# Optimization experiments

Hardware: AMD Instinct MI355X
Metric: run time of the kernel (lower is better)

## Reference

```python
import jax, jax.numpy as jnp
import numpy as np

N = 100000          # nodes
E = 1600000         # directed edges (before self-loops)
IN_FEATS = 128
HID = 16            # per-head hidden of conv1
HEADS = 8
OUT_FEATS = 128     # conv2 output (heads=1, concat=False)
K = 8               # kernel_size
M = 64              # out_channels
NEG_SLOPE_ATT = 0.2 # GATConv negative_slope
NEG_SLOPE_ACT = 0.01  # F.leaky_relu default between convs


def setup_inputs() -> dict:
    key = jax.random.key(0)
    ks = jax.random.split(key, 12)
    s = 0.1
    return {
        "x": jax.random.normal(ks[0], (N, IN_FEATS), jnp.float32),
        "edge_index": jax.random.randint(ks[1], (2, E), 0, N),
        "W1": jax.random.normal(ks[2], (IN_FEATS, HEADS * HID), jnp.float32) * s,
        "att_src1": jax.random.normal(ks[3], (HEADS, HID), jnp.float32) * s,
        "att_dst1": jax.random.normal(ks[4], (HEADS, HID), jnp.float32) * s,
        "b1": jnp.zeros((HEADS * HID,), jnp.float32),
        "W2": jax.random.normal(ks[5], (HEADS * HID, OUT_FEATS), jnp.float32) * s,
        "att_src2": jax.random.normal(ks[6], (1, OUT_FEATS), jnp.float32) * s,
        "att_dst2": jax.random.normal(ks[7], (1, OUT_FEATS), jnp.float32) * s,
        "b2": jnp.zeros((OUT_FEATS,), jnp.float32),
        "g": jax.random.normal(ks[8], (OUT_FEATS, M * K), jnp.float32) * s,
        "mu": jax.random.normal(ks[9], (K, M), jnp.float32) * s,
    }


def gat_conv(x, src, dst, W, att_src, att_dst, bias, n, heads, out_ch):
    # x: [N, F_in]; src/dst: [E'] (self-loops already appended)
    h = (x @ W).reshape(n, heads, out_ch)                 # [N, H, C]
    a_src = jnp.sum(h * att_src[None], axis=-1)           # [N, H]
    a_dst = jnp.sum(h * att_dst[None], axis=-1)           # [N, H]
    e = jax.nn.leaky_relu(a_src[src] + a_dst[dst], NEG_SLOPE_ATT)  # [E', H]
    # segment softmax over destination node (every node has a self-loop)
    e_max = jax.ops.segment_max(e, dst, num_segments=n)   # [N, H]
    e_exp = jnp.exp(e - e_max[dst])
    denom = jax.ops.segment_sum(e_exp, dst, num_segments=n)
    alpha = e_exp / (denom[dst] + 1e-16)                  # [E', H]
    msg = h[src] * alpha[:, :, None]                      # [E', H, C]
    out = jax.ops.segment_sum(msg, dst, num_segments=n)   # [N, H, C]
    return out.reshape(n, heads * out_ch) + bias


def reference(x, edge_index, W1, att_src1, att_dst1, b1,
              W2, att_src2, att_dst2, b2, g, mu):
    n = x.shape[0]
    loops = jnp.arange(n, dtype=edge_index.dtype)
    src = jnp.concatenate([edge_index[0], loops])
    dst = jnp.concatenate([edge_index[1], loops])

    h = gat_conv(x, src, dst, W1, att_src1, att_dst1, b1, n, HEADS, HID)
    h = jax.nn.leaky_relu(h, NEG_SLOPE_ACT)
    h = gat_conv(h, src, dst, W2, att_src2, att_dst2, b2, n, 1, OUT_FEATS)

    out = (h @ g).reshape(n, K, M)                        # [N, K, M]
    eps = 1e-8
    num = jnp.sum(mu[None] * out, axis=-1)                # [N, K]
    den = (jnp.maximum(jnp.linalg.norm(mu, axis=-1), eps)[None]
           * jnp.maximum(jnp.linalg.norm(out, axis=-1), eps))
    return num / den                                      # [N, K]
```

## Files before the change

### kernel.cpp

```cpp
#include <hip/hip_runtime.h>
#include <hip/hip_bf16.h>

typedef short short8 __attribute__((ext_vector_type(8)));
typedef float f32x4 __attribute__((ext_vector_type(4)));

__device__ __forceinline__ float lrelu(float x, float s) { return x > 0.f ? x : x * s; }

__device__ __forceinline__ unsigned short f2bf(float x) {
  union { __hip_bfloat16 b; unsigned short u; } cv;
  cv.b = __float2bfloat16(x);
  return cv.u;
}
__device__ __forceinline__ float bf2f(unsigned short u) {
  return __uint_as_float(((unsigned int)u) << 16);
}

__global__ void __launch_bounds__(256)
prep_kernel(const float* __restrict__ g, unsigned short* __restrict__ gt,
            const float* __restrict__ W1, const float* __restrict__ as1,
            const float* __restrict__ ad1, unsigned short* __restrict__ wt1,
            unsigned short* __restrict__ vt1,
            const float* __restrict__ W2, const float* __restrict__ as2,
            const float* __restrict__ ad2, unsigned short* __restrict__ wt2,
            unsigned short* __restrict__ vt2,
            const float* __restrict__ mu, unsigned short* __restrict__ gmt)
{
  __shared__ float ts[32][68];
  __shared__ float ss[2][128], sd[2][128];
  __shared__ float msq[8];
  const int b = blockIdx.x;
  const int t = threadIdx.x;
  if (b < 32) {
    const int kb = (b >> 3) * 32;
    const int cb = (b & 7) * 64;
    {
      const int r = t >> 3;
      const int c = (t & 7) * 8;
      float4 v0 = *(const float4*)&g[(size_t)(kb + r) * 512 + cb + c];
      float4 v1 = *(const float4*)&g[(size_t)(kb + r) * 512 + cb + c + 4];
      *(float4*)&ts[r][c] = v0;
      *(float4*)&ts[r][c + 4] = v1;
    }
    __syncthreads();
    {
      const int c = t >> 2;
      const int k0 = (t & 3) * 8;
      unsigned short pk[8];
      #pragma unroll
      for (int j = 0; j < 8; ++j) pk[j] = f2bf(ts[k0 + j][c]);
      *(short8*)&gt[(size_t)(cb + c) * 128 + kb + k0] = *(short8*)pk;
    }
  } else if (b < 160) {
    const int isW2 = (b >= 96) ? 1 : 0;
    const float* W  = isW2 ? W2 : W1;
    const float* as = isW2 ? as2 : as1;
    const float* ad = isW2 ? ad2 : ad1;
    unsigned short* wt = isW2 ? wt2 : wt1;
    unsigned short* vt = isW2 ? vt2 : vt1;
    const int HEADS = isW2 ? 1 : 8;
    const int kk = t >> 7;
    const int c  = t & 127;
    const int k  = ((b - (isW2 ? 96 : 32)) << 1) + kk;
    const float wv = W[k * 128 + c];
    wt[c * 128 + k] = f2bf(wv);
    ss[kk][c] = wv * as[c];
    sd[kk][c] = wv * ad[c];
    __syncthreads();
    if (c < 16) {
      const int C = 128 / HEADS;
      const int h = (c < 8) ? c : c - 8;
      float s = 0.f;
      if (h < HEADS) {
        const float* sb = (c < 8) ? ss[kk] : sd[kk];
        for (int j = 0; j < C; ++j) s += sb[h * C + j];
      }
      vt[c * 128 + k] = f2bf(s);
    }
  } else {
    if (t < 8) {
      float s = 0.f;
      for (int m = 0; m < 64; ++m) { const float v = mu[t * 64 + m]; s += v * v; }
      msq[t] = fmaxf(sqrtf(s), 1e-8f);
    }
    __syncthreads();
    #pragma unroll
    for (int p = 0; p < 4; ++p) {
      const int idx = t + p * 256;
      const int j = idx >> 3, k = idx & 7;
      float s = 0.f;
      for (int m = 0; m < 64; ++m) s += mu[k * 64 + m] * g[(size_t)j * 512 + k * 64 + m];
      gmt[k * 128 + j] = f2bf(s / msq[k]);
      gmt[(8 + (idx >> 7)) * 128 + (idx & 127)] = 0;
    }
  }
}

__global__ void __launch_bounds__(256)
deg_count_kernel(const int* __restrict__ edst, int* __restrict__ deg, int E, int n) {
  const int grp = blockIdx.x & 3;
  const int lo = (int)(((long long)n * grp) >> 2);
  const int hi = (int)(((long long)n * (grp + 1)) >> 2);
  const int tid = (blockIdx.x >> 2) * blockDim.x + threadIdx.x;
  const int stride = (gridDim.x >> 2) * blockDim.x;
  for (int i = tid; i < E; i += stride) {
    const int d = edst[i];
    if (d >= lo && d < hi) atomicAdd(&deg[d], 1);
  }
}

__global__ void __launch_bounds__(256)
scan1_kernel(const int* __restrict__ deg, int* __restrict__ out,
             int* __restrict__ blksum, int n) {
  __shared__ int ts[256];
  const int t = threadIdx.x;
  const int base = blockIdx.x * 2048 + t * 8;
  int v[8]; int s = 0;
  #pragma unroll
  for (int i = 0; i < 8; ++i) {
    int x = (base + i < n) ? deg[base + i] + 1 : 0;
    v[i] = s; s += x;
  }
  ts[t] = s;
  __syncthreads();
  for (int off = 1; off < 256; off <<= 1) {
    int add = (t >= off) ? ts[t - off] : 0;
    __syncthreads();
    ts[t] += add;
    __syncthreads();
  }
  const int excl = ts[t] - s;
  #pragma unroll
  for (int i = 0; i < 8; ++i)
    if (base + i < n) out[base + i] = excl + v[i];
  if (t == 255) blksum[blockIdx.x] = ts[255];
}

__global__ void scan2_kernel(int* __restrict__ blksum, int nb) {
  const int t = threadIdx.x;
  int v = (t < nb) ? blksum[t] : 0;
  #pragma unroll
  for (int off = 1; off < 64; off <<= 1) {
    int u = __shfl_up(v, off);
    if (t >= off) v += u;
  }
  if (t < nb) blksum[t] = v;
}

__global__ void scan3_kernel(int* __restrict__ out, const int* __restrict__ blksum, int n) {
  int i = blockIdx.x * blockDim.x + threadIdx.x;
  if (i >= n) return;
  int b = i >> 11;
  if (b > 0) out[i] += blksum[b - 1];
}

__global__ void __launch_bounds__(256)
scatter_kernel(const int* __restrict__ esrc, const int* __restrict__ edst,
               int* __restrict__ rowptr, int* __restrict__ col,
               int E, int n) {
  const int grp = blockIdx.x & 3;
  const int lo = (int)(((long long)n * grp) >> 2);
  const int hi = (int)(((long long)n * (grp + 1)) >> 2);
  const int tid = (blockIdx.x >> 2) * blockDim.x + threadIdx.x;
  const int stride = (gridDim.x >> 2) * blockDim.x;
  const int Etot = E + n;
  for (int i = tid; i < Etot; i += stride) {
    int s, d;
    if (i < E) { s = esrc[i]; d = edst[i]; } else { s = d = i - E; }
    if (d >= lo && d < hi) {
      int p = atomicAdd(&rowptr[d], 1);
      col[p] = s;
    }
  }
}

template<int HEADS, bool BF16IN, bool I8OUT>
__global__ void __launch_bounds__(256)
feat_mfma_kernel(const void* __restrict__ In_, const unsigned short* __restrict__ wt,
                 const unsigned short* __restrict__ vt, const float* __restrict__ bias_in,
                 void* __restrict__ Hout_, float* __restrict__ hscale,
                 float* __restrict__ a_src, float* __restrict__ a_dst, int n)
{
  __shared__ unsigned short xs[64][136];
  const int t = threadIdx.x;
  const int w = t >> 6, lane = t & 63;
  const int l15 = lane & 15, lg = lane >> 4;
  const int nbase = blockIdx.x << 6;

  {
    const int r = t >> 2;
    const int c0s = (t & 3) << 5;
    const int node = nbase + r;
    if (BF16IN) {
      const unsigned short* In2 = (const unsigned short*)In_;
      #pragma unroll
      for (int i = 0; i < 4; ++i) {
        unsigned short pk[8];
        if (node < n) {
          short8 v = *(const short8*)&In2[(size_t)node * 128 + c0s + i * 8];
          #pragma unroll
          for (int j = 0; j < 8; ++j) {
            float f = bf2f((unsigned short)v[j]) + bias_in[c0s + i * 8 + j];
            pk[j] = f2bf(lrelu(f, 0.01f));
          }
        } else {
          #pragma unroll
          for (int j = 0; j < 8; ++j) pk[j] = 0;
        }
        *(short8*)&xs[r][c0s + i * 8] = *(short8*)pk;
      }
    } else {
      const float* In1 = (const float*)In_;
      #pragma unroll
      for (int i = 0; i < 8; ++i) {
        unsigned short pk[4];
        if (node < n) {
          float4 v = *(const float4*)&In1[(size_t)node * 128 + c0s + i * 4];
          pk[0] = f2bf(v.x); pk[1] = f2bf(v.y); pk[2] = f2bf(v.z); pk[3] = f2bf(v.w);
        } else { pk[0] = pk[1] = pk[2] = pk[3] = 0; }
        *(uint2*)&xs[r][c0s + i * 4] = *(uint2*)pk;
      }
    }
  }
  __syncthreads();

  short8 afr[4];
  #pragma unroll
  for (int kc = 0; kc < 4; ++kc)
    afr[kc] = *(const short8*)&xs[w * 16 + l15][kc * 32 + lg * 8];

  const unsigned short* bp[9];
  #pragma unroll
  for (int ct = 0; ct < 8; ++ct)
    bp[ct] = wt + (size_t)(ct * 16 + l15) * 128 + lg * 8;
  bp[8] = vt + (size_t)l15 * 128 + lg * 8;

  f32x4 acc[9];
  #pragma unroll
  for (int ct = 0; ct < 9; ++ct) acc[ct] = (f32x4){0.f, 0.f, 0.f, 0.f};

  short8 bcur[9], bnxt[9];
  #pragma unroll
  for (int ct = 0; ct < 9; ++ct) bcur[ct] = *(const short8*)bp[ct];

  #pragma unroll
  for (int kc = 0; kc < 4; ++kc) {
    if (kc < 3) {
      #pragma unroll
      for (int ct = 0; ct < 9; ++ct)
        bnxt[ct] = *(const short8*)(bp[ct] + (kc + 1) * 32);
    }
    #pragma unroll
    for (int ct = 0; ct < 9; ++ct)
      acc[ct] = __builtin_amdgcn_mfma_f32_16x16x32_bf16(afr[kc], bcur[ct], acc[ct], 0, 0, 0);
    if (kc < 3) {
      #pragma unroll
      for (int ct = 0; ct < 9; ++ct) bcur[ct] = bnxt[ct];
    }
  }
  __syncthreads();

  if (I8OUT) {
    unsigned char* xb = (unsigned char*)xs;
    float inv127[4], scl[4];
    #pragma unroll
    for (int r = 0; r < 4; ++r) {
      float m = 0.f;
      #pragma unroll
      for (int ct = 0; ct < 8; ++ct) m = fmaxf(m, fabsf(acc[ct][r]));
      m = fmaxf(m, __shfl_xor(m, 1));
      m = fmaxf(m, __shfl_xor(m, 2));
      m = fmaxf(m, __shfl_xor(m, 4));
      m = fmaxf(m, __shfl_xor(m, 8));
      m = fmaxf(m, 1e-12f);
      inv127[r] = 127.f / m;
      scl[r] = m * (1.f / 127.f);
    }
    #pragma unroll
    for (int ct = 0; ct < 8; ++ct)
      #pragma unroll
      for (int r = 0; r < 4; ++r) {
        const int q = __float2int_rn(acc[ct][r] * inv127[r]);
        xb[(w * 16 + lg * 4 + r) * 272 + ct * 16 + l15] = (unsigned char)q;
      }
    if (l15 == 0) {
      #pragma unroll
      for (int r = 0; r < 4; ++r) {
        const int node = nbase + w * 16 + lg * 4 + r;
        if (node < n) hscale[node] = scl[r];
      }
    }
    __syncthreads();
    {
      const int rr = t >> 2;
      const int cc = (t & 3) * 32;
      const int node = nbase + rr;
      if (node < n) {
        unsigned char* H8 = (unsigned char*)Hout_;
        *(uint4*)&H8[(size_t)node * 128 + cc]      = *(const uint4*)&xb[rr * 272 + cc];
        *(uint4*)&H8[(size_t)node * 128 + cc + 16] = *(const uint4*)&xb[rr * 272 + cc + 16];
      }
    }
  } else {
    #pragma unroll
    for (int ct = 0; ct < 8; ++ct)
      #pragma unroll
      for (int r = 0; r < 4; ++r)
        xs[w * 16 + lg * 4 + r][ct * 16 + l15] = f2bf(acc[ct][r]);
    __syncthreads();
    {
      const int r = t >> 2;
      const int c0s = (t & 3) << 5;
      const int node = nbase + r;
      if (node < n) {
        unsigned short* Hb = (unsigned short*)Hout_;
        #pragma unroll
        for (int i = 0; i < 4; ++i)
          *(short8*)&Hb[(size_t)node * 128 + c0s + i * 8] = *(const short8*)&xs[r][c0s + i * 8];
      }
    }
  }

  #pragma unroll
  for (int r = 0; r < 4; ++r) {
    const int node = nbase + w * 16 + lg * 4 + r;
    if (node < n) {
      const float v = acc[8][r];
      if (HEADS == 8) {
        if (l15 < 8) a_src[node * 8 + l15] = v;
        else         a_dst[node * 8 + (l15 - 8)] = v;
      } else {
        if (l15 == 0) a_src[node] = v;
        else if (l15 == 8) a_dst[node] = v;
      }
    }
  }
}

template<int HEADS, bool I8H>
__global__ void __launch_bounds__(256)
agg_csr_kernel(const int* __restrict__ rowptr_end, const int* __restrict__ col,
               const float* __restrict__ a_src, const float* __restrict__ a_dst,
               const void* __restrict__ Hf_, const float* __restrict__ hscale,
               unsigned int* __restrict__ agg, int n)
{
  const int wave = threadIdx.x >> 6;
  const int lane = threadIdx.x & 63;
  const int d = blockIdx.x * 4 + wave;
  if (d >= n) return;
  const int beg = (d == 0) ? 0 : rowptr_end[d - 1];
  const int end = rowptr_end[d];

  const int ei = lane >> 3;
  const int hh = (HEADS == 8) ? (lane & 7) : 0;
  const int bh = (HEADS == 8) ? (lane >> 3) : 0;
  const float adv = (HEADS == 8) ? a_dst[d * 8 + hh] : a_dst[d];
  const unsigned int* Hu = (const unsigned int*)Hf_;
  const unsigned short* H16 = (const unsigned short*)Hf_;

  float accx = 0.f, accy = 0.f, sum = 0.f;
  const int nb8 = (end - beg) >> 3;
  int sv = 0; float a = 0.f, Sv = 0.f;
  if (nb8 > 0) {
    sv = col[beg + ei];
    a = __expf(lrelu(a_src[sv * HEADS + hh] + adv, 0.2f));
    if (I8H) Sv = hscale[sv];
    if (HEADS == 8 || (lane & 7) == 0) sum += a;
  }
  for (int b = 0; b < nb8; ++b) {
    int s[8]; float al[8];
    #pragma unroll
    for (int e = 0; e < 8; ++e) {
      s[e]  = __shfl(sv, e * 8);
      al[e] = __shfl(a, e * 8 + bh);
      if (I8H) al[e] *= __shfl(Sv, e * 8);
    }
    unsigned int hv[8];
    if (I8H) {
      #pragma unroll
      for (int e = 0; e < 8; ++e) hv[e] = H16[(size_t)s[e] * 64 + lane];
    } else {
      #pragma unroll
      for (int e = 0; e < 8; ++e) hv[e] = Hu[(size_t)s[e] * 64 + lane];
    }
    if (b + 1 < nb8) {
      sv = col[beg + ((b + 1) << 3) + ei];
      a = __expf(lrelu(a_src[sv * HEADS + hh] + adv, 0.2f));
      if (I8H) Sv = hscale[sv];
      if (HEADS == 8 || (lane & 7) == 0) sum += a;
    }
    #pragma unroll
    for (int e = 0; e < 8; ++e) {
      if (I8H) {
        const int wv = (int)hv[e];
        accx += al[e] * (float)((wv << 24) >> 24);
        accy += al[e] * (float)((wv << 16) >> 24);
      } else {
        accx += al[e] * __uint_as_float(hv[e] << 16);
        accy += al[e] * __uint_as_float(hv[e] & 0xffff0000u);
      }
    }
  }
  {
    const int p0 = beg + (nb8 << 3);
    const int cnt = end - p0;
    if (cnt > 0) {
      int svt = 0; float at = 0.f, Svt = 0.f;
      if (ei < cnt) {
        svt = col[p0 + ei];
        at = __expf(lrelu(a_src[svt * HEADS + hh] + adv, 0.2f));
        if (I8H) Svt = hscale[svt];
        if (HEADS == 8 || (lane & 7) == 0) sum += at;
      }
      for (int e = 0; e < cnt; ++e) {
        float al = __shfl(at, e * 8 + bh);
        if (I8H) al *= __shfl(Svt, e * 8);
        const int sx = __shfl(svt, e * 8);
        if (I8H) {
          const int wv = (int)H16[(size_t)sx * 64 + lane];
          accx += al * (float)((wv << 24) >> 24);
          accy += al * (float)((wv << 16) >> 24);
        } else {
          const unsigned int hv = Hu[(size_t)sx * 64 + lane];
          accx += al * __uint_as_float(hv << 16);
          accy += al * __uint_as_float(hv & 0xffff0000u);
        }
      }
    }
  }
  sum += __shfl_xor(sum, 8);
  sum += __shfl_xor(sum, 16);
  sum += __shfl_xor(sum, 32);
  const float denom = __shfl(sum, bh) + 1e-16f;
  const float inv = 1.f / denom;
  agg[(size_t)d * 64 + lane] = (unsigned int)f2bf(accx * inv) | ((unsigned int)f2bf(accy * inv) << 16);
}

__global__ void __launch_bounds__(256)
final_kernel(const unsigned short* __restrict__ agg2b, const float* __restrict__ b2,
             const unsigned short* __restrict__ gt, const unsigned short* __restrict__ gmt,
             float* __restrict__ outp, int n)
{
  __shared__ unsigned short os[32][136];
  const int t = threadIdx.x;
  const int w = t >> 6;
  const int lane = t & 63;
  const int l15 = lane & 15;
  const int lg = lane >> 4;
  const int nbase = blockIdx.x << 5;

  {
    const int r = t >> 3;
    const int c = (t & 7) * 16;
    const int node = nbase + r;
    unsigned short pk[16];
    if (node < n) {
      short8 v0 = *(const short8*)&agg2b[(size_t)node * 128 + c];
      short8 v1 = *(const short8*)&agg2b[(size_t)node * 128 + c + 8];
      #pragma unroll
      for (int j = 0; j < 8; ++j) pk[j]     = f2bf(bf2f((unsigned short)v0[j]) + b2[c + j]);
      #pragma unroll
      for (int j = 0; j < 8; ++j) pk[8 + j] = f2bf(bf2f((unsigned short)v1[j]) + b2[c + 8 + j]);
    } else {
      #pragma unroll
      for (int i = 0; i < 16; ++i) pk[i] = 0;
    }
    *(short8*)&os[r][c]     = *(short8*)&pk[0];
    *(short8*)&os[r][c + 8] = *(short8*)&pk[8];
  }
  __syncthreads();

  short8 afr[2][4];
  #pragma unroll
  for (int rt = 0; rt < 2; ++rt)
    #pragma unroll
    for (int kc = 0; kc < 4; ++kc)
      afr[rt][kc] = *(const short8*)&os[rt * 16 + l15][kc * 32 + lg * 8];

  const unsigned short* gw  = gt  + (size_t)(w * 128 + l15) * 128 + lg * 8;
  const unsigned short* gmw = gmt + (size_t)l15 * 128 + lg * 8;

  f32x4 acc[2][8];
  f32x4 accg[2];
  #pragma unroll
  for (int rt = 0; rt < 2; ++rt) {
    #pragma unroll
    for (int ct = 0; ct < 8; ++ct)
      acc[rt][ct] = (f32x4){0.f, 0.f, 0.f, 0.f};
    accg[rt] = (f32x4){0.f, 0.f, 0.f, 0.f};
  }

  short8 bcur[9], bnxt[9];
  #pragma unroll
  for (int ct = 0; ct < 8; ++ct)
    bcur[ct] = *(const short8*)&gw[(size_t)ct * 2048];
  bcur[8] = *(const short8*)gmw;

  #pragma unroll
  for (int kc = 0; kc < 4; ++kc) {
    if (kc < 3) {
      #pragma unroll
      for (int ct = 0; ct < 8; ++ct)
        bnxt[ct] = *(const short8*)&gw[(size_t)ct * 2048 + (kc + 1) * 32];
      bnxt[8] = *(const short8*)(gmw + (kc + 1) * 32);
    }
    #pragma unroll
    for (int ct = 0; ct < 8; ++ct) {
      acc[0][ct] = __builtin_amdgcn_mfma_f32_16x16x32_bf16(afr[0][kc], bcur[ct], acc[0][ct], 0, 0, 0);
      acc[1][ct] = __builtin_amdgcn_mfma_f32_16x16x32_bf16(afr[1][kc], bcur[ct], acc[1][ct], 0, 0, 0);
    }
    accg[0] = __builtin_amdgcn_mfma_f32_16x16x32_bf16(afr[0][kc], bcur[8], accg[0], 0, 0, 0);
    accg[1] = __builtin_amdgcn_mfma_f32_16x16x32_bf16(afr[1][kc], bcur[8], accg[1], 0, 0, 0);
    if (kc < 3) {
      #pragma unroll
      for (int ct = 0; ct < 9; ++ct) bcur[ct] = bnxt[ct];
    }
  }

  const int k0 = w * 2, k1 = w * 2 + 1;
  #pragma unroll
  for (int rt = 0; rt < 2; ++rt) {
    float ss0[4] = {0.f, 0.f, 0.f, 0.f};
    float ss1[4] = {0.f, 0.f, 0.f, 0.f};
    #pragma unroll
    for (int ct = 0; ct < 4; ++ct) {
      const f32x4 a = acc[rt][ct];
      const f32x4 b = acc[rt][4 + ct];
      #pragma unroll
      for (int r = 0; r < 4; ++r) {
        ss0[r] += a[r] * a[r];
        ss1[r] += b[r] * b[r];
      }
    }
    #pragma unroll
    for (int r = 0; r < 4; ++r) {
      ss0[r] += __shfl_xor(ss0[r], 1); ss1[r] += __shfl_xor(ss1[r], 1);
      ss0[r] += __shfl_xor(ss0[r], 2); ss1[r] += __shfl_xor(ss1[r], 2);
      ss0[r] += __shfl_xor(ss0[r], 4); ss1[r] += __shfl_xor(ss1[r], 4);
      ss0[r] += __shfl_xor(ss0[r], 8); ss1[r] += __shfl_xor(ss1[r], 8);
    }
    #pragma unroll
    for (int r = 0; r < 4; ++r) {
      const int node = nbase + rt * 16 + lg * 4 + r;
      if (node < n) {
        const float nv = accg[rt][r];
        if (l15 == k0)      outp[(size_t)node * 8 + k0] = nv / fmaxf(sqrtf(ss0[r]), 1e-8f);
        else if (l15 == k1) outp[(size_t)node * 8 + k1] = nv / fmaxf(sqrtf(ss1[r]), 1e-8f);
      }
    }
  }
}

extern "C" void kernel_launch(void* const* d_in, const int* in_sizes, int n_in,
                              void* d_out, int out_size, void* d_ws, size_t ws_size,
                              hipStream_t stream)
{
  const float* x   = (const float*)d_in[0];
  const int*   eix = (const int*)d_in[1];
  const float* W1  = (const float*)d_in[2];
  const float* as1 = (const float*)d_in[3];
  const float* ad1 = (const float*)d_in[4];
  const float* b1  = (const float*)d_in[5];
  const float* W2  = (const float*)d_in[6];
  const float* as2 = (const float*)d_in[7];
  const float* ad2 = (const float*)d_in[8];
  const float* b2  = (const float*)d_in[9];
  const float* g   = (const float*)d_in[10];
  const float* mu  = (const float*)d_in[11];
  float* outp = (float*)d_out;

  const int n    = in_sizes[0] / 128;
  const int E    = in_sizes[1] / 2;
  const int* esrc = eix;
  const int* edst = eix + E;

  unsigned short* hb  = (unsigned short*)d_ws;
  unsigned short* gt  = hb + (size_t)n * 128;
  unsigned short* wt1 = gt + 512 * 128;
  unsigned short* vt1 = wt1 + 128 * 128;
  unsigned short* wt2 = vt1 + 16 * 128;
  unsigned short* vt2 = wt2 + 128 * 128;
  unsigned short* gmt = vt2 + 16 * 128;
  unsigned short* agg_b = (unsigned short*)((char*)d_ws + (size_t)n * 512);
  float* asrc   = (float*)((char*)d_ws + (size_t)n * 1024);
  float* adst   = asrc + (size_t)n * 8;
  int*   rowptr = (int*)(adst + (size_t)n * 8);
  int*   col    = rowptr + n;
  float* hscale = (float*)(col + (size_t)E + n);
  int*   deg    = (int*)agg_b;
  int*   blksum = deg + n;

  prep_kernel<<<161, 256, 0, stream>>>(g, gt, W1, as1, ad1, wt1, vt1,
                                       W2, as2, ad2, wt2, vt2, mu, gmt);

  const int nb = (n + 2047) / 2048;
  hipMemsetAsync(deg, 0, (size_t)n * sizeof(int), stream);
  deg_count_kernel<<<2048, 256, 0, stream>>>(edst, deg, E, n);
  scan1_kernel<<<nb, 256, 0, stream>>>(deg, rowptr, blksum, n);
  scan2_kernel<<<1, 64, 0, stream>>>(blksum, nb);
  scan3_kernel<<<(n + 255) / 256, 256, 0, stream>>>(rowptr, blksum, n);
  scatter_kernel<<<2048, 256, 0, stream>>>(esrc, edst, rowptr, col, E, n);

  feat_mfma_kernel<8, false, true><<<(n + 63) / 64, 256, 0, stream>>>(
      x, wt1, vt1, nullptr, hb, hscale, asrc, adst, n);
  agg_csr_kernel<8, true><<<(n + 3) / 4, 256, 0, stream>>>(
      rowptr, col, asrc, adst, hb, hscale, (unsigned int*)agg_b, n);

  feat_mfma_kernel<1, true, false><<<(n + 63) / 64, 256, 0, stream>>>(
      agg_b, wt2, vt2, b1, hb, nullptr, asrc, adst, n);
  agg_csr_kernel<1, false><<<(n + 3) / 4, 256, 0, stream>>>(
      rowptr, col, asrc, adst, hb, nullptr, (unsigned int*)agg_b, n);

  final_kernel<<<(n + 31) / 32, 256, 0, stream>>>(agg_b, b2, gt, gmt, outp, n);
}
```

Before: 478.7 us.

## Merge independent kernels into shared launches to overlap CSR build with feature GEMM

Degree counting now runs as extra blocks of the weight-prep kernel, and the CSR scatter runs as extra blocks of the first feature MFMA kernel. Because the work in each merged launch is independent, atomics-bound and compute-bound blocks can run concurrently on the GPU, and two kernel launch gaps disappear. The cost is larger heterogeneous grids, where every block of the merged kernel carries the shared-memory footprint of the feature body, and the block scheduling order determines how much overlap actually happens.

```diff
diff --git a/kernel.cpp b/kernel.cpp
--- a/kernel.cpp
+++ b/kernel.cpp
@@ -14,6 +14,8 @@
 __device__ __forceinline__ float bf2f(unsigned short u) {
   return __uint_as_float(((unsigned int)u) << 16);
 }
+
+#define NSCAT 2048
 
 __global__ void __launch_bounds__(256)
 prep_kernel(const float* __restrict__ g, unsigned short* __restrict__ gt,
@@ -23,7 +25,8 @@
             const float* __restrict__ W2, const float* __restrict__ as2,
             const float* __restrict__ ad2, unsigned short* __restrict__ wt2,
             unsigned short* __restrict__ vt2,
-            const float* __restrict__ mu, unsigned short* __restrict__ gmt)
+            const float* __restrict__ mu, unsigned short* __restrict__ gmt,
+            const int* __restrict__ edst, int* __restrict__ deg, int E, int n)
 {
   __shared__ float ts[32][68];
   __shared__ float ss[2][128], sd[2][128];
@@ -76,7 +79,7 @@
       }
       vt[c * 128 + k] = f2bf(s);
     }
-  } else {
+  } else if (b == 160) {
     if (t < 8) {
       float s = 0.f;
       for (int m = 0; m < 64; ++m) { const float v = mu[t * 64 + m]; s += v * v; }
@@ -92,19 +95,17 @@
       gmt[k * 128 + j] = f2bf(s / msq[k]);
       gmt[(8 + (idx >> 7)) * 128 + (idx & 127)] = 0;
     }
-  }
-}
-
-__global__ void __launch_bounds__(256)
-deg_count_kernel(const int* __restrict__ edst, int* __restrict__ deg, int E, int n) {
-  const int grp = blockIdx.x & 3;
-  const int lo = (int)(((long long)n * grp) >> 2);
-  const int hi = (int)(((long long)n * (grp + 1)) >> 2);
-  const int tid = (blockIdx.x >> 2) * blockDim.x + threadIdx.x;
-  const int stride = (gridDim.x >> 2) * blockDim.x;
-  for (int i = tid; i < E; i += stride) {
-    const int d = edst[i];
-    if (d >= lo && d < hi) atomicAdd(&deg[d], 1);
+  } else {
+    const int bb = b - 161;
+    const int grp = bb & 3;
+    const int lo = (int)(((long long)n * grp) >> 2);
+    const int hi = (int)(((long long)n * (grp + 1)) >> 2);
+    const int tid = (bb >> 2) * blockDim.x + t;
+    const int stride = (NSCAT >> 2) * blockDim.x;
+    for (int i = tid; i < E; i += stride) {
+      const int d = edst[i];
+      if (d >= lo && d < hi) atomicAdd(&deg[d], 1);
+    }
   }
 }
 
@@ -153,15 +154,15 @@
   if (b > 0) out[i] += blksum[b - 1];
 }
 
-__global__ void __launch_bounds__(256)
-scatter_kernel(const int* __restrict__ esrc, const int* __restrict__ edst,
-               int* __restrict__ rowptr, int* __restrict__ col,
-               int E, int n) {
-  const int grp = blockIdx.x & 3;
+__device__ __forceinline__ void scatter_body(int bidx, const int* __restrict__ esrc,
+                                             const int* __restrict__ edst,
+                                             int* __restrict__ rowptr, int* __restrict__ col,
+                                             int E, int n, int tl) {
+  const int grp = bidx & 3;
   const int lo = (int)(((long long)n * grp) >> 2);
   const int hi = (int)(((long long)n * (grp + 1)) >> 2);
-  const int tid = (blockIdx.x >> 2) * blockDim.x + threadIdx.x;
-  const int stride = (gridDim.x >> 2) * blockDim.x;
+  const int tid = (bidx >> 2) * 256 + tl;
+  const int stride = (NSCAT >> 2) * 256;
   const int Etot = E + n;
   for (int i = tid; i < Etot; i += stride) {
     int s, d;
@@ -174,17 +175,17 @@
 }
 
 template<int HEADS, bool BF16IN, bool I8OUT>
-__global__ void __launch_bounds__(256)
-feat_mfma_kernel(const void* __restrict__ In_, const unsigned short* __restrict__ wt,
-                 const unsigned short* __restrict__ vt, const float* __restrict__ bias_in,
-                 void* __restrict__ Hout_, float* __restrict__ hscale,
-                 float* __restrict__ a_src, float* __restrict__ a_dst, int n)
+__device__ __forceinline__ void
+feat_body(int bidx, const void* __restrict__ In_, const unsigned short* __restrict__ wt,
+          const unsigned short* __restrict__ vt, const float* __restrict__ bias_in,
+          void* __restrict__ Hout_, float* __restrict__ hscale,
+          float* __restrict__ a_src, float* __restrict__ a_dst, int n)
 {
   __shared__ unsigned short xs[64][136];
   const int t = threadIdx.x;
   const int w = t >> 6, lane = t & 63;
   const int l15 = lane & 15, lg = lane >> 4;
-  const int nbase = blockIdx.x << 6;
+  const int nbase = bidx << 6;
 
   {
     const int r = t >> 2;
@@ -334,6 +335,31 @@
       }
     }
   }
+}
+
+__global__ void __launch_bounds__(256)
+scatter_feat1_kernel(const int* __restrict__ esrc, const int* __restrict__ edst,
+                     int* __restrict__ rowptr, int* __restrict__ col, int E,
+                     const float* __restrict__ x, const unsigned short* __restrict__ wt1,
+                     const unsigned short* __restrict__ vt1,
+                     void* __restrict__ Hout, float* __restrict__ hscale,
+                     float* __restrict__ a_src, float* __restrict__ a_dst, int n)
+{
+  if (blockIdx.x < NSCAT) {
+    scatter_body(blockIdx.x, esrc, edst, rowptr, col, E, n, threadIdx.x);
+  } else {
+    feat_body<8, false, true>(blockIdx.x - NSCAT, x, wt1, vt1, nullptr,
+                              Hout, hscale, a_src, a_dst, n);
+  }
+}
+
+__global__ void __launch_bounds__(256)
+feat2_kernel(const void* __restrict__ In_, const unsigned short* __restrict__ wt,
+             const unsigned short* __restrict__ vt, const float* __restrict__ bias_in,
+             void* __restrict__ Hout_, float* __restrict__ a_src,
+             float* __restrict__ a_dst, int n)
+{
+  feat_body<1, true, false>(blockIdx.x, In_, wt, vt, bias_in, Hout_, nullptr, a_src, a_dst, n);
 }
 
 template<int HEADS, bool I8H>
@@ -589,24 +615,24 @@
   int*   deg    = (int*)agg_b;
   int*   blksum = deg + n;
 
-  prep_kernel<<<161, 256, 0, stream>>>(g, gt, W1, as1, ad1, wt1, vt1,
-                                       W2, as2, ad2, wt2, vt2, mu, gmt);
+  hipMemsetAsync(deg, 0, (size_t)n * sizeof(int), stream);
+  prep_kernel<<<161 + NSCAT, 256, 0, stream>>>(g, gt, W1, as1, ad1, wt1, vt1,
+                                               W2, as2, ad2, wt2, vt2, mu, gmt,
+                                               edst, deg, E, n);
 
   const int nb = (n + 2047) / 2048;
-  hipMemsetAsync(deg, 0, (size_t)n * sizeof(int), stream);
-  deg_count_kernel<<<2048, 256, 0, stream>>>(edst, deg, E, n);
   scan1_kernel<<<nb, 256, 0, stream>>>(deg, rowptr, blksum, n);
   scan2_kernel<<<1, 64, 0, stream>>>(blksum, nb);
   scan3_kernel<<<(n + 255) / 256, 256, 0, stream>>>(rowptr, blksum, n);
-  scatter_kernel<<<2048, 256, 0, stream>>>(esrc, edst, rowptr, col, E, n);
-
-  feat_mfma_kernel<8, false, true><<<(n + 63) / 64, 256, 0, stream>>>(
-      x, wt1, vt1, nullptr, hb, hscale, asrc, adst, n);
+
+  const int nfeat = (n + 63) / 64;
+  scatter_feat1_kernel<<<NSCAT + nfeat, 256, 0, stream>>>(
+      esrc, edst, rowptr, col, E, x, wt1, vt1, hb, hscale, asrc, adst, n);
+
   agg_csr_kernel<8, true><<<(n + 3) / 4, 256, 0, stream>>>(
       rowptr, col, asrc, adst, hb, hscale, (unsigned int*)agg_b, n);
 
-  feat_mfma_kernel<1, true, false><<<(n + 63) / 64, 256, 0, stream>>>(
-      agg_b, wt2, vt2, b1, hb, nullptr, asrc, adst, n);
+  feat2_kernel<<<nfeat, 256, 0, stream>>>(agg_b, wt2, vt2, b1, hb, asrc, adst, n);
   agg_csr_kernel<1, false><<<(n + 3) / 4, 256, 0, stream>>>(
       rowptr, col, asrc, adst, hb, nullptr, (unsigned int*)agg_b, n);
 
```

Measured after the change: 467.5 us. 1.02x faster.
